# Optimization experiments

Hardware: AMD Instinct MI355X
Metric: run time of the kernel (lower is better)

Reference implementation:

```python
import jax, jax.numpy as jnp
import numpy as np

N_NODES = 50000
N_EDGES = 1600000
N_GRAPHS = 512
VOCAB = 1000
EMB = 32
HID = 64
N_CLASS = 2


def setup_inputs() -> dict:
    key = jax.random.key(0)
    ks = jax.random.split(key, 12)
    x_ids = jax.random.randint(ks[0], (N_NODES,), 0, VOCAB)
    edge_index = jax.random.randint(ks[1], (2, N_EDGES), 0, N_NODES)
    batch = jnp.sort(jax.random.randint(ks[2], (N_NODES,), 0, N_GRAPHS))
    def s(k, shape, fan):
        return jax.random.normal(k, shape, jnp.float32) * (1.0 / np.sqrt(fan))
    return {
        "x_ids": x_ids,
        "edge_index": edge_index,
        "batch": batch,
        "embed": s(ks[3], (VOCAB, EMB), EMB),
        "w1_l": s(ks[4], (EMB, HID), EMB),
        "b1": jnp.zeros((HID,), jnp.float32),
        "w1_r": s(ks[5], (EMB, HID), EMB),
        "w2_l": s(ks[6], (HID, HID), HID),
        "b2": jnp.zeros((HID,), jnp.float32),
        "w2_r": s(ks[7], (HID, HID), HID),
        "w_out": s(ks[8], (HID, N_CLASS), HID),
        "b_out": jnp.zeros((N_CLASS,), jnp.float32),
    }


def _sage(x, src, dst, w_l, b, w_r):
    # PyG SAGEConv (aggr='mean'): out = lin_l(mean_{j in N(i)} x_j) + lin_r(x_i)
    msg_sum = jax.ops.segment_sum(x[src], dst, num_segments=N_NODES)  # [N, d]
    deg = jax.ops.segment_sum(jnp.ones((src.shape[0],), x.dtype), dst,
                              num_segments=N_NODES)
    mean = msg_sum / jnp.maximum(deg, 1.0)[:, None]
    return mean @ w_l + b + x @ w_r


def reference(x_ids, edge_index, batch, embed, w1_l, b1, w1_r,
              w2_l, b2, w2_r, w_out, b_out):
    src, dst = edge_index[0], edge_index[1]
    x = embed[x_ids]                                  # [N, emb]
    x = jax.nn.relu(_sage(x, src, dst, w1_l, b1, w1_r))  # [N, hid]
    x = jax.nn.relu(_sage(x, src, dst, w2_l, b2, w2_r))  # [N, hid]
    # global_mean_pool over batch segments
    gsum = jax.ops.segment_sum(x, batch, num_segments=N_GRAPHS)
    gcnt = jax.ops.segment_sum(jnp.ones((N_NODES,), x.dtype), batch,
                               num_segments=N_GRAPHS)
    pooled = gsum / jnp.maximum(gcnt, 1.0)[:, None]   # [G, hid]
    return pooled @ w_out + b_out                     # [G, n_class]
```

## Files before the change

### kernel.cpp

```cpp
#include <hip/hip_runtime.h>
#include <hip/hip_bf16.h>

#define N_NODES 50000
#define N_EDGES 1600000
#define N_GRAPHS 512
#define VOCAB 1000
#define EMB 32
#define HID 64
#define N_CLASS 2

#define MAXDEG 96

#define NVEC (N_EDGES / 4)
#define SORT_VPB 1024
#define SORT_BLOCKS ((NVEC + SORT_VPB - 1) / SORT_VPB)
#define BSHIFT 8
#define BUCKET_NODES 256
#define NBUCK ((N_NODES + BUCKET_NODES - 1) / BUCKET_NODES)

#define AGG_THREADS (N_NODES * 8)
#define AGG_BLOCKS ((AGG_THREADS + 255) / 256)

#define L2P_BLOCKS 768
#define L2P_WAVES (L2P_BLOCKS * 4)
#define L2P_CHUNK ((N_NODES + L2P_WAVES - 1) / L2P_WAVES)

typedef int iv4 __attribute__((ext_vector_type(4)));
typedef unsigned short us;
typedef us usv8 __attribute__((ext_vector_type(8)));
typedef float fv4 __attribute__((ext_vector_type(4)));
typedef unsigned long long u64;

__device__ __forceinline__ float bf2f(us u) {
    union { unsigned int i; float f; } c;
    c.i = ((unsigned int)u) << 16;
    return c.f;
}
__device__ __forceinline__ us f2bf(float f) {
    union { __hip_bfloat16 b; us u; } c;
    c.b = __float2bfloat16(f);
    return c.u;
}
__device__ __forceinline__ float rdlane(float v, int k) {
    return __int_as_float(__builtin_amdgcn_readlane(__float_as_int(v), k));
}

__global__ __launch_bounds__(256) void hist_kernel(const int* __restrict__ dst,
                                                   int* __restrict__ hist) {
    __shared__ int lh[NBUCK];
    for (int b = threadIdx.x; b < NBUCK; b += 256) lh[b] = 0;
    __syncthreads();
    const iv4* dst4 = (const iv4*)dst;
    int vbase = blockIdx.x * SORT_VPB;
    #pragma unroll
    for (int t = 0; t < 4; ++t) {
        int v = vbase + t * 256 + threadIdx.x;
        if (v < NVEC) {
            iv4 d4 = __builtin_nontemporal_load(&dst4[v]);
            atomicAdd(&lh[d4.x >> BSHIFT], 1);
            atomicAdd(&lh[d4.y >> BSHIFT], 1);
            atomicAdd(&lh[d4.z >> BSHIFT], 1);
            atomicAdd(&lh[d4.w >> BSHIFT], 1);
        }
    }
    __syncthreads();
    for (int b = threadIdx.x; b < NBUCK; b += 256)
        hist[b * SORT_BLOCKS + blockIdx.x] = lh[b];
}

__global__ __launch_bounds__(256) void scan_rows_kernel(int* __restrict__ hist,
                                                        int* __restrict__ btot) {
    int* row = hist + (size_t)blockIdx.x * SORT_BLOCKS;
    __shared__ int wsum[4];
    int tid = threadIdx.x, lane = tid & 63, w = tid >> 6;
    int carry = 0;
    for (int base = 0; base < SORT_BLOCKS; base += 256) {
        int idx = base + tid;
        int v = (idx < SORT_BLOCKS) ? row[idx] : 0;
        int inc = v;
        #pragma unroll
        for (int off = 1; off < 64; off <<= 1) {
            int n = __shfl_up(inc, off, 64);
            if (lane >= off) inc += n;
        }
        if (lane == 63) wsum[w] = inc;
        __syncthreads();
        int woff = 0;
        #pragma unroll
        for (int k = 0; k < 4; ++k) if (k < w) woff += wsum[k];
        if (idx < SORT_BLOCKS) row[idx] = carry + woff + inc - v;
        carry += wsum[0] + wsum[1] + wsum[2] + wsum[3];
        __syncthreads();
    }
    if (tid == 0) btot[blockIdx.x] = carry;
}

__global__ __launch_bounds__(256) void scan_btot_kernel(const int* __restrict__ btot,
                                                        int* __restrict__ boff) {
    __shared__ int wsum[4];
    int tid = threadIdx.x, lane = tid & 63, w = tid >> 6;
    int v = (tid < NBUCK) ? btot[tid] : 0;
    int inc = v;
    #pragma unroll
    for (int off = 1; off < 64; off <<= 1) {
        int n = __shfl_up(inc, off, 64);
        if (lane >= off) inc += n;
    }
    if (lane == 63) wsum[w] = inc;
    __syncthreads();
    int woff = 0;
    #pragma unroll
    for (int k = 0; k < 4; ++k) if (k < w) woff += wsum[k];
    if (tid < NBUCK) boff[tid] = woff + inc - v;
    if (tid == 0) boff[NBUCK] = wsum[0] + wsum[1] + wsum[2] + wsum[3];
}

__global__ __launch_bounds__(256) void scatter_kernel(const int* __restrict__ src,
        const int* __restrict__ dst, const int* __restrict__ x_ids,
        const int* __restrict__ hist, const int* __restrict__ boff,
        u64* __restrict__ ebuf) {
    __shared__ int lbase[NBUCK];
    for (int b = threadIdx.x; b < NBUCK; b += 256)
        lbase[b] = hist[b * SORT_BLOCKS + blockIdx.x] + boff[b];
    __syncthreads();
    const iv4* dst4 = (const iv4*)dst;
    const iv4* src4 = (const iv4*)src;
    int vbase = blockIdx.x * SORT_VPB;
    #pragma unroll
    for (int t = 0; t < 4; ++t) {
        int v = vbase + t * 256 + threadIdx.x;
        if (v < NVEC) {
            iv4 d4 = __builtin_nontemporal_load(&dst4[v]);
            iv4 s4 = __builtin_nontemporal_load(&src4[v]);
            int pay0 = (x_ids[s4.x] << 16) | s4.x;
            int pay1 = (x_ids[s4.y] << 16) | s4.y;
            int pay2 = (x_ids[s4.z] << 16) | s4.z;
            int pay3 = (x_ids[s4.w] << 16) | s4.w;
            int p0 = atomicAdd(&lbase[d4.x >> BSHIFT], 1);
            int p1 = atomicAdd(&lbase[d4.y >> BSHIFT], 1);
            int p2 = atomicAdd(&lbase[d4.z >> BSHIFT], 1);
            int p3 = atomicAdd(&lbase[d4.w >> BSHIFT], 1);
            ebuf[p0] = ((u64)(unsigned)d4.x << 32) | (unsigned)pay0;
            ebuf[p1] = ((u64)(unsigned)d4.y << 32) | (unsigned)pay1;
            ebuf[p2] = ((u64)(unsigned)d4.z << 32) | (unsigned)pay2;
            ebuf[p3] = ((u64)(unsigned)d4.w << 32) | (unsigned)pay3;
        }
    }
}

__global__ __launch_bounds__(256) void csr_bucket_kernel(const u64* __restrict__ ebuf,
        const int* __restrict__ boff, int* __restrict__ cursor, int* __restrict__ csr) {
    int b = blockIdx.x;
    __shared__ int cur[BUCKET_NODES];
    for (int r = threadIdx.x; r < BUCKET_NODES; r += 256) cur[r] = 0;
    __syncthreads();
    int base = boff[b];
    int end  = boff[b + 1];
    int node0 = b << BSHIFT;
    for (int i = base + threadIdx.x; i < end; i += 256) {
        u64 e = ebuf[i];
        int d = (int)(e >> 32);
        int pay = (int)(e & 0xffffffffu);
        int pos = atomicAdd(&cur[d - node0], 1);
        csr[d * MAXDEG + pos] = pay;
    }
    __syncthreads();
    for (int r = threadIdx.x; r < BUCKET_NODES; r += 256) {
        int d = node0 + r;
        if (d < N_NODES) cursor[d] = cur[r];
    }
}

__global__ void precompute_e1_kernel(const float* __restrict__ embed,
                                     const float* __restrict__ w1l,
                                     const float* __restrict__ w1r,
                                     us* __restrict__ e1b,
                                     float* __restrict__ e1r) {
    int id = blockIdx.x * blockDim.x + threadIdx.x;
    if (id >= VOCAB * HID) return;
    int v = id >> 6, j = id & 63;
    float a = 0.0f, b = 0.0f;
    #pragma unroll
    for (int k = 0; k < EMB; ++k) {
        float ev = embed[v * EMB + k];
        a = fmaf(ev, w1l[k * HID + j], a);
        b = fmaf(ev, w1r[k * HID + j], b);
    }
    e1b[id] = f2bf(a);
    e1r[id] = b;
}

__global__ __launch_bounds__(256) void agg1_lin1_kernel(
        const int* __restrict__ x_ids, const int* __restrict__ csr,
        const int* __restrict__ deg_arr, const us* __restrict__ e1b,
        const float* __restrict__ e1r, const float* __restrict__ b1,
        float* __restrict__ h1, us* __restrict__ h1b) {
    int tid = blockIdx.x * blockDim.x + threadIdx.x;
    int lane = threadIdx.x & 63;
    int g = lane >> 3, c8 = lane & 7;
    int node = (tid >> 6) * 8 + g;
    bool valid = node < N_NODES;
    int nclamp = valid ? node : 0;
    int deg = valid ? deg_arr[nclamp] : 0;
    const int* crow = csr + (size_t)nclamp * MAXDEG;
    float a0=0.f,a1=0.f,a2=0.f,a3=0.f,a4=0.f,a5=0.f,a6=0.f,a7=0.f;
    for (int k = 0; k < deg; k += 4) {
        iv4 cv = *(const iv4*)(crow + k);
        #define GATH1(CVAL, T)                                                   \
        if (k + (T) < deg) {                                                     \
            int cls = (CVAL) >> 16;                                              \
            usv8 r = *(const usv8*)(e1b + cls * HID + c8 * 8);                   \
            a0 += bf2f(r[0]); a1 += bf2f(r[1]); a2 += bf2f(r[2]); a3 += bf2f(r[3]); \
            a4 += bf2f(r[4]); a5 += bf2f(r[5]); a6 += bf2f(r[6]); a7 += bf2f(r[7]); \
        }
        GATH1(cv.x, 0) GATH1(cv.y, 1) GATH1(cv.z, 2) GATH1(cv.w, 3)
        #undef GATH1
    }
    if (!valid) return;
    float inv = 1.0f / fmaxf((float)deg, 1.0f);
    int xid = x_ids[nclamp];
    const fv4* er = (const fv4*)(e1r + xid * HID + c8 * 8);
    fv4 e0 = er[0], e1v = er[1];
    const fv4* bb = (const fv4*)(b1 + c8 * 8);
    fv4 b0 = bb[0], b1v = bb[1];
    fv4 h0, h1v;
    h0.x = fmaxf(a0 * inv + b0.x + e0.x, 0.0f);
    h0.y = fmaxf(a1 * inv + b0.y + e0.y, 0.0f);
    h0.z = fmaxf(a2 * inv + b0.z + e0.z, 0.0f);
    h0.w = fmaxf(a3 * inv + b0.w + e0.w, 0.0f);
    h1v.x = fmaxf(a4 * inv + b1v.x + e1v.x, 0.0f);
    h1v.y = fmaxf(a5 * inv + b1v.y + e1v.y, 0.0f);
    h1v.z = fmaxf(a6 * inv + b1v.z + e1v.z, 0.0f);
    h1v.w = fmaxf(a7 * inv + b1v.w + e1v.w, 0.0f);
    int o = node * HID + c8 * 8;
    *(fv4*)(h1 + o) = h0;
    *(fv4*)(h1 + o + 4) = h1v;
    usv8 hb;
    hb[0] = f2bf(h0.x); hb[1] = f2bf(h0.y); hb[2] = f2bf(h0.z); hb[3] = f2bf(h0.w);
    hb[4] = f2bf(h1v.x); hb[5] = f2bf(h1v.y); hb[6] = f2bf(h1v.z); hb[7] = f2bf(h1v.w);
    *(usv8*)(h1b + o) = hb;
}

__global__ __launch_bounds__(256) void agg2_mean_kernel(
        const us* __restrict__ h1b, const int* __restrict__ csr,
        const int* __restrict__ deg_arr, float* __restrict__ mean2) {
    int tid = blockIdx.x * blockDim.x + threadIdx.x;
    int lane = threadIdx.x & 63;
    int g = lane >> 3, c8 = lane & 7;
    int node = (tid >> 6) * 8 + g;
    bool valid = node < N_NODES;
    int nclamp = valid ? node : 0;
    int deg = valid ? deg_arr[nclamp] : 0;
    const int* crow = csr + (size_t)nclamp * MAXDEG;
    float a0=0.f,a1=0.f,a2=0.f,a3=0.f,a4=0.f,a5=0.f,a6=0.f,a7=0.f;
    for (int k = 0; k < deg; k += 4) {
        iv4 cv = *(const iv4*)(crow + k);
        #define GATH2(CVAL, T)                                                   \
        if (k + (T) < deg) {                                                     \
            int nb = (CVAL) & 0xFFFF;                                            \
            usv8 r = *(const usv8*)(h1b + nb * HID + c8 * 8);                    \
            a0 += bf2f(r[0]); a1 += bf2f(r[1]); a2 += bf2f(r[2]); a3 += bf2f(r[3]); \
            a4 += bf2f(r[4]); a5 += bf2f(r[5]); a6 += bf2f(r[6]); a7 += bf2f(r[7]); \
        }
        GATH2(cv.x, 0) GATH2(cv.y, 1) GATH2(cv.z, 2) GATH2(cv.w, 3)
        #undef GATH2
    }
    if (!valid) return;
    float inv = 1.0f / fmaxf((float)deg, 1.0f);
    fv4 m0, m1;
    m0.x = a0 * inv; m0.y = a1 * inv; m0.z = a2 * inv; m0.w = a3 * inv;
    m1.x = a4 * inv; m1.y = a5 * inv; m1.z = a6 * inv; m1.w = a7 * inv;
    int o = node * HID + c8 * 8;
    *(fv4*)(mean2 + o) = m0;
    *(fv4*)(mean2 + o + 4) = m1;
}

__global__ __launch_bounds__(256) void lin2_pool_kernel(
        const float* __restrict__ mean2, const float* __restrict__ h1,
        const float* __restrict__ w2l, const float* __restrict__ b2,
        const float* __restrict__ w2r, const int* __restrict__ batch,
        float* __restrict__ gsum) {
    int lane = threadIdx.x & 63;
    int wv = (blockIdx.x * blockDim.x + threadIdx.x) >> 6;
    int i0 = wv * L2P_CHUNK;
    int i1 = i0 + L2P_CHUNK; if (i1 > N_NODES) i1 = N_NODES;
    if (i0 >= N_NODES) return;
    float wl[HID], wr[HID];
    #pragma unroll
    for (int k = 0; k < HID; ++k) {
        wl[k] = w2l[k * HID + lane];
        wr[k] = w2r[k * HID + lane];
    }
    float bj = b2[lane];
    int curg = __builtin_amdgcn_readfirstlane(batch[i0]);
    float accp = 0.0f;
    float m = mean2[i0 * HID + lane];
    float h = h1[i0 * HID + lane];
    for (int i = i0; i < i1; ++i) {
        float mn = 0.f, hn = 0.f;
        if (i + 1 < i1) {
            mn = mean2[(i + 1) * HID + lane];
            hn = h1[(i + 1) * HID + lane];
        }
        int g = __builtin_amdgcn_readfirstlane(batch[i]);
        if (g != curg) {
            atomicAdd(&gsum[curg * HID + lane], accp);
            accp = 0.0f;
            curg = g;
        }
        float z = bj;
        #pragma unroll
        for (int k = 0; k < HID; ++k)
            z = fmaf(rdlane(m, k), wl[k], fmaf(rdlane(h, k), wr[k], z));
        accp += fmaxf(z, 0.0f);
        m = mn; h = hn;
    }
    atomicAdd(&gsum[curg * HID + lane], accp);
}

__global__ void out_kernel(const float* __restrict__ gsum, const int* __restrict__ batch,
                           const float* __restrict__ w_out, const float* __restrict__ b_out,
                           float* __restrict__ out) {
    int id = blockIdx.x * blockDim.x + threadIdx.x;
    if (id >= N_GRAPHS * N_CLASS) return;
    int g = id >> 1, c = id & 1;
    int lo = 0, hi = N_NODES;
    while (lo < hi) { int mid = (lo + hi) >> 1; if (batch[mid] < g) lo = mid + 1; else hi = mid; }
    int first = lo;
    lo = 0; hi = N_NODES;
    while (lo < hi) { int mid = (lo + hi) >> 1; if (batch[mid] <= g) lo = mid + 1; else hi = mid; }
    float cnt = (float)(lo - first);
    float inv = 1.0f / fmaxf(cnt, 1.0f);
    float acc = b_out[c];
    #pragma unroll
    for (int j = 0; j < HID; ++j)
        acc = fmaf(gsum[g * HID + j] * inv, w_out[j * N_CLASS + c], acc);
    out[id] = acc;
}


extern "C" void kernel_launch(void* const* d_in, const int* in_sizes, int n_in,
                              void* d_out, int out_size, void* d_ws, size_t ws_size,
                              hipStream_t stream) {
    const int*   x_ids = (const int*)d_in[0];
    const int*   edge  = (const int*)d_in[1];
    const int*   batch = (const int*)d_in[2];
    const float* embed = (const float*)d_in[3];
    const float* w1l   = (const float*)d_in[4];
    const float* b1    = (const float*)d_in[5];
    const float* w1r   = (const float*)d_in[6];
    const float* w2l   = (const float*)d_in[7];
    const float* b2    = (const float*)d_in[8];
    const float* w2r   = (const float*)d_in[9];
    const float* wout  = (const float*)d_in[10];
    const float* bout  = (const float*)d_in[11];
    const int* src = edge;
    const int* dst = edge + N_EDGES;
    float* out = (float*)d_out;

    char* ws = (char*)d_ws;
    size_t off = 0;
    auto alloc = [&](size_t bytes) -> void* {
        void* p = ws + off;
        off += (bytes + 255) & ~(size_t)255;
        return p;
    };
    float*  h1     = (float*)alloc((size_t)N_NODES * HID * 4);
    us*     h1b    = (us*)alloc((size_t)N_NODES * HID * 2);
    float*  mean2  = (float*)alloc((size_t)N_NODES * HID * 4);
    int*    csr    = (int*)alloc((size_t)N_NODES * MAXDEG * 4);
    int*    cursor = (int*)alloc((size_t)N_NODES * 4);
    int*    hist   = (int*)alloc((size_t)NBUCK * SORT_BLOCKS * 4);
    int*    btot   = (int*)alloc((size_t)NBUCK * 4);
    int*    boff   = (int*)alloc((size_t)(NBUCK + 1) * 4);
    us*     e1b    = (us*)alloc((size_t)VOCAB * HID * 2);
    float*  e1r    = (float*)alloc((size_t)VOCAB * HID * 4);
    float*  gsum   = (float*)alloc((size_t)N_GRAPHS * HID * 4);

    u64* ebuf = (u64*)mean2;

    hipMemsetAsync(gsum, 0, (size_t)N_GRAPHS * HID * 4, stream);

    const int B = 256;
    precompute_e1_kernel<<<(VOCAB * HID + B - 1) / B, B, 0, stream>>>(embed, w1l, w1r, e1b, e1r);

    hist_kernel<<<SORT_BLOCKS, B, 0, stream>>>(dst, hist);
    scan_rows_kernel<<<NBUCK, B, 0, stream>>>(hist, btot);
    scan_btot_kernel<<<1, B, 0, stream>>>(btot, boff);
    scatter_kernel<<<SORT_BLOCKS, B, 0, stream>>>(src, dst, x_ids, hist, boff, ebuf);
    csr_bucket_kernel<<<NBUCK, B, 0, stream>>>(ebuf, boff, cursor, csr);

    agg1_lin1_kernel<<<AGG_BLOCKS, B, 0, stream>>>(x_ids, csr, cursor,
                                                   e1b, e1r, b1, h1, h1b);
    agg2_mean_kernel<<<AGG_BLOCKS, B, 0, stream>>>(h1b, csr, cursor, mean2);
    lin2_pool_kernel<<<L2P_BLOCKS, B, 0, stream>>>(mean2, h1, w2l, b2, w2r, batch, gsum);
    out_kernel<<<(N_GRAPHS * N_CLASS + B - 1) / B, B, 0, stream>>>(gsum, batch, wout, bout, out);
}
```

Baseline: 223.2 us.

## Fuse graph pipeline kernels: merge precompute, scan, CSR build, and aggregation stages

Merges the embedding-projection precompute into the histogram launch and folds the bucket-offset scan into every scatter block. The CSR bucket build is fused with layer-1 aggregation through a shared-memory adjacency copy, with smaller buckets so that copy fits in LDS. Layer-2 mean aggregation is fused with lin2 and pooling via shared memory, which removes the mean2 buffer round-trip. gsum zeroing moves into a kernel, so one memset and several launches go away. The costs are a redundant scan in every scatter block, lower occupancy from the large LDS array, and a smaller per-wave pooling chunk that issues more atomics.

```diff
diff --git a/kernel.cpp b/kernel.cpp
--- a/kernel.cpp
+++ b/kernel.cpp
@@ -14,16 +14,12 @@
 #define NVEC (N_EDGES / 4)
 #define SORT_VPB 1024
 #define SORT_BLOCKS ((NVEC + SORT_VPB - 1) / SORT_VPB)
-#define BSHIFT 8
-#define BUCKET_NODES 256
+#define BSHIFT 7
+#define BUCKET_NODES 128
 #define NBUCK ((N_NODES + BUCKET_NODES - 1) / BUCKET_NODES)
-
-#define AGG_THREADS (N_NODES * 8)
-#define AGG_BLOCKS ((AGG_THREADS + 255) / 256)
-
-#define L2P_BLOCKS 768
-#define L2P_WAVES (L2P_BLOCKS * 4)
-#define L2P_CHUNK ((N_NODES + L2P_WAVES - 1) / L2P_WAVES)
+#define CSR_LSTR 100
+
+#define E1_BLOCKS ((VOCAB * HID + 255) / 256)
 
 typedef int iv4 __attribute__((ext_vector_type(4)));
 typedef unsigned short us;
@@ -45,27 +41,45 @@
     return __int_as_float(__builtin_amdgcn_readlane(__float_as_int(v), k));
 }
 
-__global__ __launch_bounds__(256) void hist_kernel(const int* __restrict__ dst,
-                                                   int* __restrict__ hist) {
+__global__ __launch_bounds__(256) void pre_hist_kernel(
+        const int* __restrict__ dst, int* __restrict__ hist,
+        const float* __restrict__ embed, const float* __restrict__ w1l,
+        const float* __restrict__ w1r, us* __restrict__ e1b,
+        float* __restrict__ e1r) {
     __shared__ int lh[NBUCK];
-    for (int b = threadIdx.x; b < NBUCK; b += 256) lh[b] = 0;
-    __syncthreads();
-    const iv4* dst4 = (const iv4*)dst;
-    int vbase = blockIdx.x * SORT_VPB;
-    #pragma unroll
-    for (int t = 0; t < 4; ++t) {
-        int v = vbase + t * 256 + threadIdx.x;
-        if (v < NVEC) {
-            iv4 d4 = __builtin_nontemporal_load(&dst4[v]);
-            atomicAdd(&lh[d4.x >> BSHIFT], 1);
-            atomicAdd(&lh[d4.y >> BSHIFT], 1);
-            atomicAdd(&lh[d4.z >> BSHIFT], 1);
-            atomicAdd(&lh[d4.w >> BSHIFT], 1);
-        }
-    }
-    __syncthreads();
-    for (int b = threadIdx.x; b < NBUCK; b += 256)
-        hist[b * SORT_BLOCKS + blockIdx.x] = lh[b];
+    if (blockIdx.x < SORT_BLOCKS) {
+        for (int b = threadIdx.x; b < NBUCK; b += 256) lh[b] = 0;
+        __syncthreads();
+        const iv4* dst4 = (const iv4*)dst;
+        int vbase = blockIdx.x * SORT_VPB;
+        #pragma unroll
+        for (int t = 0; t < 4; ++t) {
+            int v = vbase + t * 256 + threadIdx.x;
+            if (v < NVEC) {
+                iv4 d4 = __builtin_nontemporal_load(&dst4[v]);
+                atomicAdd(&lh[d4.x >> BSHIFT], 1);
+                atomicAdd(&lh[d4.y >> BSHIFT], 1);
+                atomicAdd(&lh[d4.z >> BSHIFT], 1);
+                atomicAdd(&lh[d4.w >> BSHIFT], 1);
+            }
+        }
+        __syncthreads();
+        for (int b = threadIdx.x; b < NBUCK; b += 256)
+            hist[b * SORT_BLOCKS + blockIdx.x] = lh[b];
+    } else {
+        int id = (blockIdx.x - SORT_BLOCKS) * 256 + threadIdx.x;
+        if (id >= VOCAB * HID) return;
+        int v = id >> 6, j = id & 63;
+        float a = 0.0f, b = 0.0f;
+        #pragma unroll
+        for (int k = 0; k < EMB; ++k) {
+            float ev = embed[v * EMB + k];
+            a = fmaf(ev, w1l[k * HID + j], a);
+            b = fmaf(ev, w1r[k * HID + j], b);
+        }
+        e1b[id] = f2bf(a);
+        e1r[id] = b;
+    }
 }
 
 __global__ __launch_bounds__(256) void scan_rows_kernel(int* __restrict__ hist,
@@ -95,33 +109,37 @@
     if (tid == 0) btot[blockIdx.x] = carry;
 }
 
-__global__ __launch_bounds__(256) void scan_btot_kernel(const int* __restrict__ btot,
-                                                        int* __restrict__ boff) {
+__global__ __launch_bounds__(256) void scatter_kernel(const int* __restrict__ src,
+        const int* __restrict__ dst, const int* __restrict__ x_ids,
+        const int* __restrict__ hist, const int* __restrict__ btot,
+        int* __restrict__ boff, u64* __restrict__ ebuf) {
+    __shared__ int lbase[NBUCK];
     __shared__ int wsum[4];
     int tid = threadIdx.x, lane = tid & 63, w = tid >> 6;
-    int v = (tid < NBUCK) ? btot[tid] : 0;
-    int inc = v;
-    #pragma unroll
-    for (int off = 1; off < 64; off <<= 1) {
-        int n = __shfl_up(inc, off, 64);
-        if (lane >= off) inc += n;
-    }
-    if (lane == 63) wsum[w] = inc;
-    __syncthreads();
-    int woff = 0;
-    #pragma unroll
-    for (int k = 0; k < 4; ++k) if (k < w) woff += wsum[k];
-    if (tid < NBUCK) boff[tid] = woff + inc - v;
-    if (tid == 0) boff[NBUCK] = wsum[0] + wsum[1] + wsum[2] + wsum[3];
-}
-
-__global__ __launch_bounds__(256) void scatter_kernel(const int* __restrict__ src,
-        const int* __restrict__ dst, const int* __restrict__ x_ids,
-        const int* __restrict__ hist, const int* __restrict__ boff,
-        u64* __restrict__ ebuf) {
-    __shared__ int lbase[NBUCK];
-    for (int b = threadIdx.x; b < NBUCK; b += 256)
-        lbase[b] = hist[b * SORT_BLOCKS + blockIdx.x] + boff[b];
+    int carry = 0;
+    for (int base = 0; base < NBUCK; base += 256) {
+        int idx = base + tid;
+        int v = (idx < NBUCK) ? btot[idx] : 0;
+        int inc = v;
+        #pragma unroll
+        for (int off = 1; off < 64; off <<= 1) {
+            int n = __shfl_up(inc, off, 64);
+            if (lane >= off) inc += n;
+        }
+        if (lane == 63) wsum[w] = inc;
+        __syncthreads();
+        int woff = 0;
+        #pragma unroll
+        for (int k = 0; k < 4; ++k) if (k < w) woff += wsum[k];
+        if (idx < NBUCK) lbase[idx] = carry + woff + inc - v;
+        carry += wsum[0] + wsum[1] + wsum[2] + wsum[3];
+        __syncthreads();
+    }
+    for (int b = tid; b < NBUCK; b += 256) {
+        if (blockIdx.x == 0) boff[b] = lbase[b];
+        lbase[b] += hist[b * SORT_BLOCKS + blockIdx.x];
+    }
+    if (blockIdx.x == 0 && tid == 0) boff[NBUCK] = carry;
     __syncthreads();
     const iv4* dst4 = (const iv4*)dst;
     const iv4* src4 = (const iv4*)src;
@@ -148,143 +166,94 @@
     }
 }
 
-__global__ __launch_bounds__(256) void csr_bucket_kernel(const u64* __restrict__ ebuf,
-        const int* __restrict__ boff, int* __restrict__ cursor, int* __restrict__ csr) {
+__global__ __launch_bounds__(256) void csr_agg1_kernel(const u64* __restrict__ ebuf,
+        const int* __restrict__ boff, int* __restrict__ cursor, int* __restrict__ csr,
+        const int* __restrict__ x_ids, const us* __restrict__ e1b,
+        const float* __restrict__ e1r, const float* __restrict__ b1,
+        float* __restrict__ h1, us* __restrict__ h1b, float* __restrict__ gsum) {
+    __shared__ int csr_l[BUCKET_NODES * CSR_LSTR];
+    __shared__ int cur[BUCKET_NODES];
     int b = blockIdx.x;
-    __shared__ int cur[BUCKET_NODES];
-    for (int r = threadIdx.x; r < BUCKET_NODES; r += 256) cur[r] = 0;
+    int tid = threadIdx.x;
+    for (int r = tid; r < BUCKET_NODES; r += 256) cur[r] = 0;
+    if (b < 128) gsum[b * 256 + tid] = 0.0f;
     __syncthreads();
     int base = boff[b];
     int end  = boff[b + 1];
     int node0 = b << BSHIFT;
-    for (int i = base + threadIdx.x; i < end; i += 256) {
+    for (int i = base + tid; i < end; i += 256) {
         u64 e = ebuf[i];
         int d = (int)(e >> 32);
         int pay = (int)(e & 0xffffffffu);
-        int pos = atomicAdd(&cur[d - node0], 1);
-        csr[d * MAXDEG + pos] = pay;
+        int r = d - node0;
+        int pos = atomicAdd(&cur[r], 1);
+        csr_l[r * CSR_LSTR + pos] = pay;
+        csr[(size_t)d * MAXDEG + pos] = pay;
     }
     __syncthreads();
-    for (int r = threadIdx.x; r < BUCKET_NODES; r += 256) {
+    for (int r = tid; r < BUCKET_NODES; r += 256) {
         int d = node0 + r;
         if (d < N_NODES) cursor[d] = cur[r];
     }
-}
-
-__global__ void precompute_e1_kernel(const float* __restrict__ embed,
-                                     const float* __restrict__ w1l,
-                                     const float* __restrict__ w1r,
-                                     us* __restrict__ e1b,
-                                     float* __restrict__ e1r) {
-    int id = blockIdx.x * blockDim.x + threadIdx.x;
-    if (id >= VOCAB * HID) return;
-    int v = id >> 6, j = id & 63;
-    float a = 0.0f, b = 0.0f;
-    #pragma unroll
-    for (int k = 0; k < EMB; ++k) {
-        float ev = embed[v * EMB + k];
-        a = fmaf(ev, w1l[k * HID + j], a);
-        b = fmaf(ev, w1r[k * HID + j], b);
-    }
-    e1b[id] = f2bf(a);
-    e1r[id] = b;
-}
-
-__global__ __launch_bounds__(256) void agg1_lin1_kernel(
-        const int* __restrict__ x_ids, const int* __restrict__ csr,
-        const int* __restrict__ deg_arr, const us* __restrict__ e1b,
-        const float* __restrict__ e1r, const float* __restrict__ b1,
-        float* __restrict__ h1, us* __restrict__ h1b) {
-    int tid = blockIdx.x * blockDim.x + threadIdx.x;
-    int lane = threadIdx.x & 63;
+    int lane = tid & 63;
+    int wv = tid >> 6;
     int g = lane >> 3, c8 = lane & 7;
-    int node = (tid >> 6) * 8 + g;
-    bool valid = node < N_NODES;
-    int nclamp = valid ? node : 0;
-    int deg = valid ? deg_arr[nclamp] : 0;
-    const int* crow = csr + (size_t)nclamp * MAXDEG;
-    float a0=0.f,a1=0.f,a2=0.f,a3=0.f,a4=0.f,a5=0.f,a6=0.f,a7=0.f;
-    for (int k = 0; k < deg; k += 4) {
-        iv4 cv = *(const iv4*)(crow + k);
-        #define GATH1(CVAL, T)                                                   \
-        if (k + (T) < deg) {                                                     \
-            int cls = (CVAL) >> 16;                                              \
-            usv8 r = *(const usv8*)(e1b + cls * HID + c8 * 8);                   \
-            a0 += bf2f(r[0]); a1 += bf2f(r[1]); a2 += bf2f(r[2]); a3 += bf2f(r[3]); \
-            a4 += bf2f(r[4]); a5 += bf2f(r[5]); a6 += bf2f(r[6]); a7 += bf2f(r[7]); \
-        }
-        GATH1(cv.x, 0) GATH1(cv.y, 1) GATH1(cv.z, 2) GATH1(cv.w, 3)
-        #undef GATH1
-    }
-    if (!valid) return;
-    float inv = 1.0f / fmaxf((float)deg, 1.0f);
-    int xid = x_ids[nclamp];
-    const fv4* er = (const fv4*)(e1r + xid * HID + c8 * 8);
-    fv4 e0 = er[0], e1v = er[1];
-    const fv4* bb = (const fv4*)(b1 + c8 * 8);
-    fv4 b0 = bb[0], b1v = bb[1];
-    fv4 h0, h1v;
-    h0.x = fmaxf(a0 * inv + b0.x + e0.x, 0.0f);
-    h0.y = fmaxf(a1 * inv + b0.y + e0.y, 0.0f);
-    h0.z = fmaxf(a2 * inv + b0.z + e0.z, 0.0f);
-    h0.w = fmaxf(a3 * inv + b0.w + e0.w, 0.0f);
-    h1v.x = fmaxf(a4 * inv + b1v.x + e1v.x, 0.0f);
-    h1v.y = fmaxf(a5 * inv + b1v.y + e1v.y, 0.0f);
-    h1v.z = fmaxf(a6 * inv + b1v.z + e1v.z, 0.0f);
-    h1v.w = fmaxf(a7 * inv + b1v.w + e1v.w, 0.0f);
-    int o = node * HID + c8 * 8;
-    *(fv4*)(h1 + o) = h0;
-    *(fv4*)(h1 + o + 4) = h1v;
-    usv8 hb;
-    hb[0] = f2bf(h0.x); hb[1] = f2bf(h0.y); hb[2] = f2bf(h0.z); hb[3] = f2bf(h0.w);
-    hb[4] = f2bf(h1v.x); hb[5] = f2bf(h1v.y); hb[6] = f2bf(h1v.z); hb[7] = f2bf(h1v.w);
-    *(usv8*)(h1b + o) = hb;
-}
-
-__global__ __launch_bounds__(256) void agg2_mean_kernel(
-        const us* __restrict__ h1b, const int* __restrict__ csr,
-        const int* __restrict__ deg_arr, float* __restrict__ mean2) {
-    int tid = blockIdx.x * blockDim.x + threadIdx.x;
-    int lane = threadIdx.x & 63;
-    int g = lane >> 3, c8 = lane & 7;
-    int node = (tid >> 6) * 8 + g;
-    bool valid = node < N_NODES;
-    int nclamp = valid ? node : 0;
-    int deg = valid ? deg_arr[nclamp] : 0;
-    const int* crow = csr + (size_t)nclamp * MAXDEG;
-    float a0=0.f,a1=0.f,a2=0.f,a3=0.f,a4=0.f,a5=0.f,a6=0.f,a7=0.f;
-    for (int k = 0; k < deg; k += 4) {
-        iv4 cv = *(const iv4*)(crow + k);
-        #define GATH2(CVAL, T)                                                   \
-        if (k + (T) < deg) {                                                     \
-            int nb = (CVAL) & 0xFFFF;                                            \
-            usv8 r = *(const usv8*)(h1b + nb * HID + c8 * 8);                    \
-            a0 += bf2f(r[0]); a1 += bf2f(r[1]); a2 += bf2f(r[2]); a3 += bf2f(r[3]); \
-            a4 += bf2f(r[4]); a5 += bf2f(r[5]); a6 += bf2f(r[6]); a7 += bf2f(r[7]); \
-        }
-        GATH2(cv.x, 0) GATH2(cv.y, 1) GATH2(cv.z, 2) GATH2(cv.w, 3)
-        #undef GATH2
-    }
-    if (!valid) return;
-    float inv = 1.0f / fmaxf((float)deg, 1.0f);
-    fv4 m0, m1;
-    m0.x = a0 * inv; m0.y = a1 * inv; m0.z = a2 * inv; m0.w = a3 * inv;
-    m1.x = a4 * inv; m1.y = a5 * inv; m1.z = a6 * inv; m1.w = a7 * inv;
-    int o = node * HID + c8 * 8;
-    *(fv4*)(mean2 + o) = m0;
-    *(fv4*)(mean2 + o + 4) = m1;
-}
-
-__global__ __launch_bounds__(256) void lin2_pool_kernel(
-        const float* __restrict__ mean2, const float* __restrict__ h1,
+    for (int slot = wv * 8 + g; slot < BUCKET_NODES; slot += 32) {
+        int node = node0 + slot;
+        bool valid = node < N_NODES;
+        int deg = valid ? cur[slot] : 0;
+        const int* crow = csr_l + slot * CSR_LSTR;
+        float a0=0.f,a1=0.f,a2=0.f,a3=0.f,a4=0.f,a5=0.f,a6=0.f,a7=0.f;
+        for (int k = 0; k < deg; k += 4) {
+            iv4 cv = *(const iv4*)(crow + k);
+            #define GATH1(CVAL, T)                                                   \
+            if (k + (T) < deg) {                                                     \
+                int cls = (CVAL) >> 16;                                              \
+                usv8 r = *(const usv8*)(e1b + cls * HID + c8 * 8);                   \
+                a0 += bf2f(r[0]); a1 += bf2f(r[1]); a2 += bf2f(r[2]); a3 += bf2f(r[3]); \
+                a4 += bf2f(r[4]); a5 += bf2f(r[5]); a6 += bf2f(r[6]); a7 += bf2f(r[7]); \
+            }
+            GATH1(cv.x, 0) GATH1(cv.y, 1) GATH1(cv.z, 2) GATH1(cv.w, 3)
+            #undef GATH1
+        }
+        if (!valid) continue;
+        float inv = 1.0f / fmaxf((float)deg, 1.0f);
+        int xid = x_ids[node];
+        const fv4* er = (const fv4*)(e1r + xid * HID + c8 * 8);
+        fv4 e0 = er[0], e1v = er[1];
+        const fv4* bb = (const fv4*)(b1 + c8 * 8);
+        fv4 b0 = bb[0], b1v = bb[1];
+        fv4 h0, h1v;
+        h0.x = fmaxf(a0 * inv + b0.x + e0.x, 0.0f);
+        h0.y = fmaxf(a1 * inv + b0.y + e0.y, 0.0f);
+        h0.z = fmaxf(a2 * inv + b0.z + e0.z, 0.0f);
+        h0.w = fmaxf(a3 * inv + b0.w + e0.w, 0.0f);
+        h1v.x = fmaxf(a4 * inv + b1v.x + e1v.x, 0.0f);
+        h1v.y = fmaxf(a5 * inv + b1v.y + e1v.y, 0.0f);
+        h1v.z = fmaxf(a6 * inv + b1v.z + e1v.z, 0.0f);
+        h1v.w = fmaxf(a7 * inv + b1v.w + e1v.w, 0.0f);
+        int o = node * HID + c8 * 8;
+        *(fv4*)(h1 + o) = h0;
+        *(fv4*)(h1 + o + 4) = h1v;
+        usv8 hb;
+        hb[0] = f2bf(h0.x); hb[1] = f2bf(h0.y); hb[2] = f2bf(h0.z); hb[3] = f2bf(h0.w);
+        hb[4] = f2bf(h1v.x); hb[5] = f2bf(h1v.y); hb[6] = f2bf(h1v.z); hb[7] = f2bf(h1v.w);
+        *(usv8*)(h1b + o) = hb;
+    }
+}
+
+__global__ __launch_bounds__(256) void agg2_lin2_kernel(
+        const us* __restrict__ h1b, const float* __restrict__ h1,
+        const int* __restrict__ csr, const int* __restrict__ deg_arr,
         const float* __restrict__ w2l, const float* __restrict__ b2,
         const float* __restrict__ w2r, const int* __restrict__ batch,
         float* __restrict__ gsum) {
-    int lane = threadIdx.x & 63;
-    int wv = (blockIdx.x * blockDim.x + threadIdx.x) >> 6;
-    int i0 = wv * L2P_CHUNK;
-    int i1 = i0 + L2P_CHUNK; if (i1 > N_NODES) i1 = N_NODES;
-    if (i0 >= N_NODES) return;
+    __shared__ float msh[4][8][64];
+    int tid = threadIdx.x;
+    int lane = tid & 63;
+    int wv = tid >> 6;
+    int wave_g = (blockIdx.x * 256 + tid) >> 6;
+    int n0 = wave_g * 8;
     float wl[HID], wr[HID];
     #pragma unroll
     for (int k = 0; k < HID; ++k) {
@@ -292,28 +261,51 @@
         wr[k] = w2r[k * HID + lane];
     }
     float bj = b2[lane];
-    int curg = __builtin_amdgcn_readfirstlane(batch[i0]);
+    if (n0 < N_NODES) {
+        int g = lane >> 3, c8 = lane & 7;
+        int node = n0 + g;
+        int deg = deg_arr[node];
+        const int* crow = csr + (size_t)node * MAXDEG;
+        float a0=0.f,a1=0.f,a2=0.f,a3=0.f,a4=0.f,a5=0.f,a6=0.f,a7=0.f;
+        for (int k = 0; k < deg; k += 4) {
+            iv4 cv = *(const iv4*)(crow + k);
+            #define GATH2(CVAL, T)                                                   \
+            if (k + (T) < deg) {                                                     \
+                int nb = (CVAL) & 0xFFFF;                                            \
+                usv8 r = *(const usv8*)(h1b + nb * HID + c8 * 8);                    \
+                a0 += bf2f(r[0]); a1 += bf2f(r[1]); a2 += bf2f(r[2]); a3 += bf2f(r[3]); \
+                a4 += bf2f(r[4]); a5 += bf2f(r[5]); a6 += bf2f(r[6]); a7 += bf2f(r[7]); \
+            }
+            GATH2(cv.x, 0) GATH2(cv.y, 1) GATH2(cv.z, 2) GATH2(cv.w, 3)
+            #undef GATH2
+        }
+        float inv = 1.0f / fmaxf((float)deg, 1.0f);
+        fv4 m0, m1;
+        m0.x = a0 * inv; m0.y = a1 * inv; m0.z = a2 * inv; m0.w = a3 * inv;
+        m1.x = a4 * inv; m1.y = a5 * inv; m1.z = a6 * inv; m1.w = a7 * inv;
+        *(fv4*)&msh[wv][g][c8 * 8] = m0;
+        *(fv4*)&msh[wv][g][c8 * 8 + 4] = m1;
+    }
+    __syncthreads();
+    if (n0 >= N_NODES) return;
+    int curg = __builtin_amdgcn_readfirstlane(batch[n0]);
     float accp = 0.0f;
-    float m = mean2[i0 * HID + lane];
-    float h = h1[i0 * HID + lane];
-    for (int i = i0; i < i1; ++i) {
-        float mn = 0.f, hn = 0.f;
-        if (i + 1 < i1) {
-            mn = mean2[(i + 1) * HID + lane];
-            hn = h1[(i + 1) * HID + lane];
-        }
-        int g = __builtin_amdgcn_readfirstlane(batch[i]);
-        if (g != curg) {
+    #pragma unroll
+    for (int t = 0; t < 8; ++t) {
+        int node = n0 + t;
+        float m = msh[wv][t][lane];
+        float h = h1[node * HID + lane];
+        int gg = __builtin_amdgcn_readfirstlane(batch[node]);
+        if (gg != curg) {
             atomicAdd(&gsum[curg * HID + lane], accp);
             accp = 0.0f;
-            curg = g;
+            curg = gg;
         }
         float z = bj;
         #pragma unroll
         for (int k = 0; k < HID; ++k)
             z = fmaf(rdlane(m, k), wl[k], fmaf(rdlane(h, k), wr[k], z));
         accp += fmaxf(z, 0.0f);
-        m = mn; h = hn;
     }
     atomicAdd(&gsum[curg * HID + lane], accp);
 }
@@ -367,7 +359,7 @@
     };
     float*  h1     = (float*)alloc((size_t)N_NODES * HID * 4);
     us*     h1b    = (us*)alloc((size_t)N_NODES * HID * 2);
-    float*  mean2  = (float*)alloc((size_t)N_NODES * HID * 4);
+    u64*    ebuf   = (u64*)alloc((size_t)N_EDGES * 8);
     int*    csr    = (int*)alloc((size_t)N_NODES * MAXDEG * 4);
     int*    cursor = (int*)alloc((size_t)N_NODES * 4);
     int*    hist   = (int*)alloc((size_t)NBUCK * SORT_BLOCKS * 4);
@@ -377,22 +369,14 @@
     float*  e1r    = (float*)alloc((size_t)VOCAB * HID * 4);
     float*  gsum   = (float*)alloc((size_t)N_GRAPHS * HID * 4);
 
-    u64* ebuf = (u64*)mean2;
-
-    hipMemsetAsync(gsum, 0, (size_t)N_GRAPHS * HID * 4, stream);
-
     const int B = 256;
-    precompute_e1_kernel<<<(VOCAB * HID + B - 1) / B, B, 0, stream>>>(embed, w1l, w1r, e1b, e1r);
-
-    hist_kernel<<<SORT_BLOCKS, B, 0, stream>>>(dst, hist);
+    pre_hist_kernel<<<SORT_BLOCKS + E1_BLOCKS, B, 0, stream>>>(dst, hist,
+                                                               embed, w1l, w1r, e1b, e1r);
     scan_rows_kernel<<<NBUCK, B, 0, stream>>>(hist, btot);
-    scan_btot_kernel<<<1, B, 0, stream>>>(btot, boff);
-    scatter_kernel<<<SORT_BLOCKS, B, 0, stream>>>(src, dst, x_ids, hist, boff, ebuf);
-    csr_bucket_kernel<<<NBUCK, B, 0, stream>>>(ebuf, boff, cursor, csr);
-
-    agg1_lin1_kernel<<<AGG_BLOCKS, B, 0, stream>>>(x_ids, csr, cursor,
-                                                   e1b, e1r, b1, h1, h1b);
-    agg2_mean_kernel<<<AGG_BLOCKS, B, 0, stream>>>(h1b, csr, cursor, mean2);
-    lin2_pool_kernel<<<L2P_BLOCKS, B, 0, stream>>>(mean2, h1, w2l, b2, w2r, batch, gsum);
+    scatter_kernel<<<SORT_BLOCKS, B, 0, stream>>>(src, dst, x_ids, hist, btot, boff, ebuf);
+    csr_agg1_kernel<<<NBUCK, B, 0, stream>>>(ebuf, boff, cursor, csr,
+                                             x_ids, e1b, e1r, b1, h1, h1b, gsum);
+    agg2_lin2_kernel<<<(N_NODES / 8 + 3) / 4, B, 0, stream>>>(h1b, h1, csr, cursor,
+                                                              w2l, b2, w2r, batch, gsum);
     out_kernel<<<(N_GRAPHS * N_CLASS + B - 1) / B, B, 0, stream>>>(gsum, batch, wout, bout, out);
 }
```

Result: slower. 255.7 us (+14.6%).
